# Kernel tuning notes

Measured on AMD Instinct MI355X. Metric: run time of the kernel, lower is better.

Reference implementation:

```python
import jax, jax.numpy as jnp
import numpy as np

GRID_RES = 96

TRIANGLE_TABLE = jnp.array([
    [-1, -1, -1, -1, -1, -1], [1, 0, 2, -1, -1, -1], [4, 0, 3, -1, -1, -1], [1, 4, 2, 1, 3, 4],
    [3, 1, 5, -1, -1, -1], [2, 3, 0, 2, 5, 3], [1, 4, 0, 1, 5, 4], [4, 2, 5, -1, -1, -1],
    [4, 5, 2, -1, -1, -1], [4, 1, 0, 4, 5, 1], [3, 2, 0, 3, 5, 2], [1, 3, 5, -1, -1, -1],
    [4, 1, 2, 4, 3, 1], [3, 0, 4, -1, -1, -1], [2, 0, 1, -1, -1, -1], [-1, -1, -1, -1, -1, -1]],
    dtype=jnp.int32)
NUM_TRIANGLES_TABLE = jnp.array([0, 1, 1, 2, 1, 2, 2, 1, 1, 2, 2, 1, 2, 1, 1, 0], dtype=jnp.int32)
BASE_TET_EDGES = jnp.array([0, 1, 0, 2, 0, 3, 1, 2, 1, 3, 2, 3], dtype=jnp.int32)


def _build_tet_grid(R):
    # vertices on an (R+1)^3 lattice spanning [-0.5, 0.5]^3
    n = R + 1
    lin = np.linspace(-0.5, 0.5, n, dtype=np.float32)
    X, Y, Z = np.meshgrid(lin, lin, lin, indexing='ij')
    verts = np.stack([X, Y, Z], axis=-1).reshape(-1, 3)
    idx = np.arange(n ** 3, dtype=np.int32).reshape(n, n, n)
    corners = []
    for dx in (0, 1):
        for dy in (0, 1):
            for dz in (0, 1):
                corners.append(idx[dx:dx + R, dy:dy + R, dz:dz + R].reshape(-1))
    c = np.stack(corners, axis=-1)  # (R^3, 8); corner bit order = dx*4 + dy*2 + dz
    SIX_TETS = np.array([[0, 5, 1, 7], [0, 1, 3, 7], [0, 3, 2, 7],
                         [0, 2, 6, 7], [0, 6, 4, 7], [0, 4, 5, 7]], dtype=np.int32)
    tets = c[:, SIX_TETS].reshape(-1, 4)  # (6*R^3, 4)
    return verts, tets


def _map_uv(face_gidx, max_idx):
    N = int(np.ceil(np.sqrt((max_idx + 1) // 2)))
    lin = jnp.linspace(0.0, 1.0 - 1.0 / N, N, dtype=jnp.float32)
    tex_y, tex_x = jnp.meshgrid(lin, lin, indexing='ij')
    pad = 0.9 / N
    uvs = jnp.stack([tex_x, tex_y, tex_x + pad, tex_y,
                     tex_x + pad, tex_y + pad, tex_x, tex_y + pad], axis=-1).reshape(-1, 2)
    tq = face_gidx // 2
    tet_idx = (tq // N) * N + (tq % N)
    tri_idx = face_gidx % 2
    uv_idx = jnp.stack([tet_idx * 4, tet_idx * 4 + tri_idx + 1, tet_idx * 4 + tri_idx + 2],
                       axis=-1).reshape(-1, 3)
    return uvs, uv_idx


def setup_inputs() -> dict:
    verts_np, tets_np = _build_tet_grid(GRID_RES)
    key = jax.random.key(0)
    verts = jnp.asarray(verts_np)
    noise = jax.random.normal(key, (verts.shape[0],), dtype=jnp.float32) * 0.02
    sdf_n = 0.35 - jnp.linalg.norm(verts, axis=-1) + noise  # sphere SDF + noise
    # 6 features per vertex: deformed position (xyz) + color (rgb=0.5), as in getMesh
    pos_nx3 = jnp.concatenate([verts, jnp.full(verts.shape, 0.5, dtype=jnp.float32)], axis=-1)
    return {"pos_nx3": pos_nx3, "sdf_n": sdf_n, "tet_fx4": jnp.asarray(tets_np)}


def reference(pos_nx3, sdf_n, tet_fx4):
    occ_n = sdf_n >= 0
    occ_fx4 = occ_n[tet_fx4]                       # (F, 4)
    occ_sum = occ_fx4.sum(-1)
    valid = (occ_sum > 0) & (occ_sum < 4)
    vt = tet_fx4[valid]                            # (T, 4) surface-crossing tets

    all_edges = vt[:, BASE_TET_EDGES].reshape(-1, 2)
    all_edges = jnp.sort(all_edges, axis=1)        # == sort_edges (min, max)
    unique_edges, idx_map = jnp.unique(all_edges, axis=0, return_inverse=True)
    idx_map = idx_map.reshape(-1)

    mask_edges = occ_n[unique_edges].sum(-1) == 1  # sign-crossing edges
    # mapping[mask] = arange(num_crossing); else -1 (cumsum assigns in sorted order)
    mapping = jnp.where(mask_edges, jnp.cumsum(mask_edges.astype(jnp.int32)) - 1, -1)
    idx_map = mapping[idx_map].reshape(-1, 6)      # (T, 6)
    interp_v = unique_edges[mask_edges]            # (Nv, 2)

    e_pos = pos_nx3[interp_v]                      # (Nv, 2, 6)
    e_sdf = sdf_n[interp_v] * jnp.array([1.0, -1.0], dtype=sdf_n.dtype)  # negate 2nd
    denom = e_sdf.sum(1, keepdims=True)            # (Nv, 1)
    w = jnp.flip(e_sdf, axis=1) / denom            # (Nv, 2) interpolation weights
    verts = (e_pos * w[..., None]).sum(1)          # (Nv, 6)

    v_id = jnp.array([1, 2, 4, 8], dtype=jnp.int32)
    tetindex = (occ_fx4[valid].astype(jnp.int32) * v_id).sum(-1)
    num_tri = NUM_TRIANGLES_TABLE[tetindex]
    tt = TRIANGLE_TABLE[tetindex]
    m1 = num_tri == 1
    m2 = num_tri == 2
    faces1 = jnp.take_along_axis(idx_map[m1], tt[m1][:, :3], axis=1).reshape(-1, 3)
    faces2 = jnp.take_along_axis(idx_map[m2], tt[m2][:, :6], axis=1).reshape(-1, 3)
    faces = jnp.concatenate([faces1, faces2], axis=0)

    num_tets = tet_fx4.shape[0]
    tet_gidx = jnp.arange(num_tets, dtype=jnp.int32)[valid]
    g2 = tet_gidx[m2] * 2
    face_gidx = jnp.concatenate([tet_gidx[m1] * 2,
                                 jnp.stack([g2, g2 + 1], axis=-1).reshape(-1)], axis=0)
    uvs, uv_idx = _map_uv(face_gidx, num_tets * 2)
    return verts, faces, uvs, uv_idx
```

## Files before the change

### kernel.cpp

```cpp
#include <hip/hip_runtime.h>
#include <stdint.h>

#define N1     97
#define N1SQ   9409
#define NV3    912673
#define RES    96
#define NCELL  884736
#define NCOLS  9409
#define COLS_PER_BLK 8
#define NBLK1  1177
#define SEG    2
#define UVFLOATS 42467328

#define VB2 3566
#define FB2 3456
#define NSPARSE (VB2 + FB2)
#define UVB2 10368
#define P2BLOCKS (2 * NSPARSE + (UVB2 - NSPARSE))

typedef float f4v __attribute__((ext_vector_type(4)));

__device__ __constant__ int d_tt[16][6] = {
    {-1,-1,-1,-1,-1,-1}, {1,0,2,-1,-1,-1}, {4,0,3,-1,-1,-1}, {1,4,2,1,3,4},
    {3,1,5,-1,-1,-1}, {2,3,0,2,5,3}, {1,4,0,1,5,4}, {4,2,5,-1,-1,-1},
    {4,5,2,-1,-1,-1}, {4,1,0,4,5,1}, {3,2,0,3,5,2}, {1,3,5,-1,-1,-1},
    {4,1,2,4,3,1}, {3,0,4,-1,-1,-1}, {2,0,1,-1,-1,-1}, {-1,-1,-1,-1,-1,-1}};
__device__ __constant__ int d_six[6][4] = {
    {0,5,1,7},{0,1,3,7},{0,3,2,7},{0,2,6,7},{0,6,4,7},{0,4,5,7}};
__device__ __constant__ int d_eb[6][2] = {{0,1},{0,2},{0,3},{1,2},{1,3},{2,3}};
__device__ __constant__ int d_diroff[7] = {1, 97, 98, 9409, 9410, 9506, 9507};

__device__ __forceinline__ int corner_off(int b) {
    return (b >> 2) * N1SQ + ((b >> 1) & 1) * N1 + (b & 1);
}

__device__ __forceinline__ float uvval(uint32_t p) {
    uint32_t cell = p >> 3;
    uint32_t k = p & 7u;
    uint32_t i = cell / 2304u;
    uint32_t j = cell - i * 2304u;
    uint32_t idx = (k & 1u) ? i : j;
    bool addpad = (k & 1u) ? (k >= 5u) : (k == 2u || k == 4u);
    return (float)idx * (1.0f / 2304.0f) + (addpad ? 0.9f / 2304.0f : 0.0f);
}

__global__ __launch_bounds__(1024) void k_p1(const float* __restrict__ sdf,
                                             uint8_t* __restrict__ mask,
                                             uint16_t* __restrict__ vloc,
                                             uint32_t* __restrict__ vsums,
                                             uint8_t* __restrict__ cocc,
                                             uint32_t* __restrict__ cloc,
                                             uint64_t* __restrict__ csums) {
    __shared__ uint8_t  sgn[COLS_PER_BLK][128];
    __shared__ uint64_t wtc[16];
    int t = threadIdx.x;
    int lane = t & 63, wv = t >> 6;
    int bid = blockIdx.x;
    int sub = t >> 7, z = t & 127;
    int col = bid * COLS_PER_BLK + sub;
    bool vcol = col < NCOLS;
    int x = 0, y = 0;
    if (vcol) { x = col / N1; y = col - x * N1; }
    bool bx = x < RES, by = y < RES, bz = z < RES;
    bool vact = vcol && (z < N1);
    int b00 = col * N1;
    float f00 = 0.f, f01 = 0.f, f10 = 0.f, f11 = 0.f;
    if (vact) {
        f00 = sdf[b00 + z];
        if (by) f01 = sdf[b00 + N1 + z];
        if (bx) f10 = sdf[b00 + N1SQ + z];
        if (bx && by) f11 = sdf[b00 + N1SQ + N1 + z];
    }
    uint32_t sb = (f00 >= 0.f ? 1u : 0u) | (f01 >= 0.f ? 2u : 0u) |
                  (f10 >= 0.f ? 4u : 0u) | (f11 >= 0.f ? 8u : 0u);
    sgn[sub][z] = (uint8_t)sb;
    __syncthreads();
    uint32_t s1 = bz ? (uint32_t)sgn[sub][z + 1] : 0u;

    uint32_t o0 = sb & 1u;
    uint32_t vm = 0;
    if (vact) {
        if (bz && ((s1 & 1u) != o0)) vm |= 1u;
        if (by && (((sb >> 1) & 1u) != o0)) vm |= 2u;
        if (by && bz && (((s1 >> 1) & 1u) != o0)) vm |= 4u;
        if (bx && (((sb >> 2) & 1u) != o0)) vm |= 8u;
        if (bx && bz && (((s1 >> 2) & 1u) != o0)) vm |= 16u;
        if (bx && by && (((sb >> 3) & 1u) != o0)) vm |= 32u;
        if (bx && by && bz && (((s1 >> 3) & 1u) != o0)) vm |= 64u;
    }
    uint32_t cnt = __popc(vm);
    bool cact = vact && bx && by && bz;
    uint32_t occ = 0, m1 = 0, m2 = 0;
    if (cact) {
        occ = (sb & 1u) | ((s1 & 1u) << 1) | (((sb >> 1) & 1u) << 2) | (((s1 >> 1) & 1u) << 3) |
              (((sb >> 2) & 1u) << 4) | (((s1 >> 2) & 1u) << 5) |
              (((sb >> 3) & 1u) << 6) | (((s1 >> 3) & 1u) << 7);
        if (occ != 0u && occ != 255u) {
#pragma unroll
            for (int k = 0; k < 6; k++) {
                int ti = ((occ >> d_six[k][0]) & 1) | (((occ >> d_six[k][1]) & 1) << 1) |
                         (((occ >> d_six[k][2]) & 1) << 2) | (((occ >> d_six[k][3]) & 1) << 3);
                int pc = __popc((uint32_t)ti);
                m1 += (pc == 1 || pc == 3) ? 1u : 0u;
                m2 += (pc == 2) ? 1u : 0u;
            }
        }
    }
    uint64_t val = (uint64_t)(cnt | (m1 << 16)) | ((uint64_t)m2 << 32);
    unsigned long long incl = val;
#pragma unroll
    for (int d = 1; d < 64; d <<= 1) {
        unsigned long long u = __shfl_up(incl, d, 64);
        if (lane >= d) incl += u;
    }
    if (lane == 63) wtc[wv] = incl;
    __syncthreads();
    uint64_t pre = 0;
#pragma unroll
    for (int w = 0; w < 16; w++)
        if (w < wv) pre += wtc[w];
    uint64_t excl = pre + (uint64_t)incl - val;

    if (vact) {
        mask[b00 + z] = (uint8_t)vm;
        vloc[b00 + z] = (uint16_t)(excl & 0xffffu);
    }
    if (cact) {
        int c = (x * RES + y) * RES + z;
        cocc[c] = (uint8_t)occ;
        cloc[c] = (uint32_t)((excl >> 16) & 0xffffu) | ((uint32_t)((excl >> 32) & 0xffffu) << 16);
    }
    if (t == 0) {
        uint64_t btot = 0;
#pragma unroll
        for (int w = 0; w < 16; w++) btot += wtc[w];
        vsums[bid] = (uint32_t)(btot & 0xffffu);
        csums[bid] = ((btot >> 16) & 0xffffu) | (((btot >> 32) & 0xffffu) << 32);
    }
}

__global__ __launch_bounds__(1024) void k_sums2(uint32_t* __restrict__ vsums,
                                                uint64_t* __restrict__ csums,
                                                uint32_t* __restrict__ tot) {
    __shared__ uint32_t wtv[16];
    __shared__ uint64_t wtc[16];
    int t = threadIdx.x;
    int lane = t & 63, wv = t >> 6;
    uint32_t sv = 0; uint64_t sc = 0;
    int base = t * SEG;
#pragma unroll
    for (int j = 0; j < SEG; j++) {
        int idx = base + j;
        if (idx < NBLK1) { sv += vsums[idx]; sc += csums[idx]; }
    }
    uint32_t iv = sv; unsigned long long ic = sc;
#pragma unroll
    for (int d = 1; d < 64; d <<= 1) {
        uint32_t u1 = __shfl_up(iv, d, 64);
        unsigned long long u2 = __shfl_up(ic, d, 64);
        if (lane >= d) { iv += u1; ic += u2; }
    }
    if (lane == 63) { wtv[wv] = iv; wtc[wv] = ic; }
    __syncthreads();
    uint32_t pv = 0; uint64_t pc2 = 0;
#pragma unroll
    for (int w = 0; w < 16; w++)
        if (w < wv) { pv += wtv[w]; pc2 += wtc[w]; }
    uint32_t rv = pv + iv - sv;
    uint64_t rc = pc2 + (uint64_t)ic - sc;
#pragma unroll
    for (int j = 0; j < SEG; j++) {
        int idx = base + j;
        if (idx < NBLK1) {
            uint32_t a = vsums[idx]; uint64_t b = csums[idx];
            vsums[idx] = rv; csums[idx] = rc;
            rv += a; rc += b;
        }
    }
    if (t == 0) {
        uint32_t NV = 0; uint64_t tc = 0;
#pragma unroll
        for (int w = 0; w < 16; w++) { NV += wtv[w]; tc += wtc[w]; }
        uint32_t NF1 = (uint32_t)(tc & 0xffffffffu);
        uint32_t NF2 = (uint32_t)(tc >> 32);
        uint32_t NF  = NF1 + 2u * NF2;
        tot[0] = NV; tot[1] = NF1; tot[2] = NF2;
        tot[3] = NV * 6u;
        tot[4] = NV * 6u + NF * 3u;
        tot[5] = NV * 6u + NF * 3u + UVFLOATS;
    }
}

__global__ __launch_bounds__(256) void k_p2(const float* __restrict__ sdf,
                                            const float* __restrict__ pos,
                                            const uint8_t* __restrict__ mask,
                                            const uint16_t* __restrict__ vloc,
                                            const uint32_t* __restrict__ vsums,
                                            const uint8_t* __restrict__ cocc,
                                            const uint32_t* __restrict__ cloc,
                                            const uint64_t* __restrict__ csums,
                                            const uint32_t* __restrict__ tot,
                                            float* __restrict__ out) {
    __shared__ uint2 ls[4][768];
    int bid = blockIdx.x;
    int t = threadIdx.x;
    int lane = t & 63, wv = t >> 6;
    int sparse = -1, uvb = -1;
    if (bid < 2 * NSPARSE) {
        if (bid & 1) uvb = bid >> 1;
        else sparse = bid >> 1;
    } else {
        uvb = NSPARSE + (bid - 2 * NSPARSE);
    }

    if (uvb >= 0) {
        uint32_t tot4 = tot[4];
        uint32_t A = (tot4 + 3u) & ~3u;
        uint32_t end = tot4 + UVFLOATS;
        uint32_t nvec = (end - A) >> 2;
        uint32_t vi0 = (uint32_t)uvb * 1024u + (uint32_t)t;
        uint32_t p0 = (A - tot4) + vi0 * 4u;
        uint32_t cell = p0 >> 3;
        uint32_t ph4 = p0 & 4u;
        uint32_t i = cell / 2304u;
        uint32_t j = cell - i * 2304u;
        const float s = 1.0f / 2304.0f, pd = 0.9f / 2304.0f;
#pragma unroll
        for (int rr = 0; rr < 4; rr++) {
            uint32_t vi = vi0 + (uint32_t)rr * 256u;
            if (vi < nvec) {
                float xx = (float)j * s, yy = (float)i * s;
                f4v val;
                if (ph4) { val.x = xx + pd; val.y = yy + pd; val.z = xx;      val.w = yy + pd; }
                else     { val.x = xx;      val.y = yy;      val.z = xx + pd; val.w = yy; }
                *(f4v*)(out + A + (size_t)vi * 4u) = val;
            }
            j += 128u;
            if (j >= 2304u) { j -= 2304u; i += 1u; }
        }
        if (uvb == 0 && t == 0) {
            for (uint32_t e = tot4; e < A; e++) out[e] = uvval(e - tot4);
            for (uint32_t e = A + nvec * 4u; e < end; e++) out[e] = uvval(e - tot4);
        }
        return;
    }

    if (sparse < VB2) {
        int v = sparse * 256 + wv * 64 + lane;
        uint32_t m = (v < NV3) ? (uint32_t)mask[v] : 0u;
        uint32_t cnt = __popc(m);
        uint32_t incl = cnt;
#pragma unroll
        for (int d = 1; d < 64; d <<= 1) {
            uint32_t u = __shfl_up(incl, d, 64);
            if (lane >= d) incl += u;
        }
        uint32_t E = __shfl(incl, 63);
        if (E == 0) return;
        uint32_t slot = incl - cnt;
        if (cnt) {
            uint32_t gvid = (uint32_t)vloc[v] + vsums[(v / N1) >> 3];
#pragma unroll
            for (int d = 0; d < 7; d++) {
                if ((m >> d) & 1u) {
                    ls[wv][slot] = make_uint2((uint32_t)v, (gvid << 3) | (uint32_t)d);
                    gvid++; slot++;
                }
            }
        }
        for (uint32_t j = lane; j < E; j += 64) {
            uint2 e = ls[wv][j];
            uint32_t v0 = e.x;
            uint32_t dir = e.y & 7u;
            uint32_t vid = e.y >> 3;
            uint32_t b = v0 + (uint32_t)d_diroff[dir];
            float sa = sdf[v0];
            float sbv = sdf[b];
            float inv = 1.0f / (sa - sbv);
            float w0 = -sbv * inv;
            float w1 = sa * inv;
            const float2* pa2 = (const float2*)(pos + (size_t)v0 * 6);
            const float2* pb2 = (const float2*)(pos + (size_t)b * 6);
            float2* o2 = (float2*)(out + (size_t)vid * 6);
#pragma unroll
            for (int k = 0; k < 3; k++) {
                float2 a = pa2[k], bb = pb2[k];
                float2 o;
                o.x = a.x * w0 + bb.x * w1;
                o.y = a.y * w0 + bb.y * w1;
                o2[k] = o;
            }
        }
        return;
    }

    {
        int c = (sparse - VB2) * 256 + wv * 64 + lane;
        uint32_t occ = cocc[c];
        bool valid = (occ != 0u && occ != 255u);
        uint32_t NF1 = tot[1];
        uint32_t tis = 0, nts = 0, cnt = 0;
        if (valid) {
#pragma unroll
            for (int k = 0; k < 6; k++) {
                int ti = ((occ >> d_six[k][0]) & 1) | (((occ >> d_six[k][1]) & 1) << 1) |
                         (((occ >> d_six[k][2]) & 1) << 2) | (((occ >> d_six[k][3]) & 1) << 3);
                int pc = __popc((uint32_t)ti);
                int nt = (pc == 2) ? 2 : ((pc == 1 || pc == 3) ? 1 : 0);
                tis |= (uint32_t)ti << (4 * k);
                nts |= (uint32_t)nt << (2 * k);
                cnt += (uint32_t)nt;
            }
        }
        uint32_t incl = cnt;
#pragma unroll
        for (int d = 1; d < 64; d <<= 1) {
            uint32_t u = __shfl_up(incl, d, 64);
            if (lane >= d) incl += u;
        }
        uint32_t E = __shfl(incl, 63);
        if (E == 0) return;
        uint32_t slot = incl - cnt;
        if (cnt) {
            uint32_t cl = cloc[c];
            uint64_t cs = csums[(((c / (RES * RES)) * N1) + ((c / RES) % RES)) >> 3];
            uint32_t r1 = (uint32_t)(cs & 0xffffffffu) + (cl & 0xffffu);
            uint32_t r2 = (uint32_t)(cs >> 32) + (cl >> 16);
#pragma unroll 1
            for (int k = 0; k < 6; k++) {
                uint32_t nt = (nts >> (2 * k)) & 3u;
                if (!nt) continue;
                uint32_t ti = (tis >> (4 * k)) & 15u;
                uint32_t row0;
                if (nt == 1) { row0 = r1; r1++; }
                else         { row0 = NF1 + 2u * r2; r2++; }
                for (uint32_t tri = 0; tri < nt; tri++) {
                    ls[wv][slot] = make_uint2((uint32_t)c,
                        ((row0 + tri) << 8) | (ti << 4) | ((uint32_t)k << 1) | tri);
                    slot++;
                }
            }
        }
        uint32_t fbase = tot[3];
        uint32_t ubase = tot[5];
        for (uint32_t j = lane; j < E; j += 64) {
            uint2 e = ls[wv][j];
            uint32_t cc = e.x;
            uint32_t tri = e.y & 1u;
            uint32_t k = (e.y >> 1) & 7u;
            uint32_t ti = (e.y >> 4) & 15u;
            uint32_t rr = e.y >> 8;
            uint32_t cx = cc / (RES * RES);
            uint32_t r0 = cc - cx * (RES * RES);
            uint32_t cy = r0 / RES;
            uint32_t cz = r0 - cy * RES;
            int base = (int)(cx * N1SQ + cy * N1 + cz);
            float* f = out + (size_t)fbase + (size_t)rr * 3;
            float* u = out + (size_t)ubase + (size_t)rr * 3;
#pragma unroll
            for (int jj = 0; jj < 3; jj++) {
                int ee = d_tt[ti][tri * 3 + jj];
                int c0 = d_six[k][d_eb[ee][0]];
                int c1 = d_six[k][d_eb[ee][1]];
                int bl = c0 & c1;
                int rank = (c0 ^ c1) - 1;
                int v0 = base + corner_off(bl);
                uint32_t vid = (uint32_t)vloc[v0] + vsums[(v0 / N1) >> 3] +
                               (uint32_t)__popc((uint32_t)mask[v0] & ((1u << rank) - 1u));
                f[jj] = (float)vid;
            }
            uint32_t t_g = cc * 6u + k;
            u[0] = (float)(4u * t_g);
            u[1] = (float)(4u * t_g + tri + 1u);
            u[2] = (float)(4u * t_g + tri + 2u);
        }
    }
}

extern "C" void kernel_launch(void* const* d_in, const int* in_sizes, int n_in,
                              void* d_out, int out_size, void* d_ws, size_t ws_size,
                              hipStream_t stream) {
    const float* pos = (const float*)d_in[0];
    const float* sdf = (const float*)d_in[1];
    float* out = (float*)d_out;

    uint8_t* ws = (uint8_t*)d_ws;
    size_t off = 0;
    auto alloc = [&](size_t bytes) {
        void* p = ws + off;
        off = (off + bytes + 255) & ~(size_t)255;
        return p;
    };
    uint32_t* tot   = (uint32_t*)alloc(64);
    uint8_t*  mask  = (uint8_t*)alloc(NV3);
    uint16_t* vloc  = (uint16_t*)alloc((size_t)NV3 * 2);
    uint32_t* vsums = (uint32_t*)alloc((size_t)NBLK1 * 4);
    uint8_t*  cocc  = (uint8_t*)alloc(NCELL);
    uint32_t* cloc  = (uint32_t*)alloc((size_t)NCELL * 4);
    uint64_t* csums = (uint64_t*)alloc((size_t)NBLK1 * 8);

    hipLaunchKernelGGL(k_p1, dim3(NBLK1), dim3(1024), 0, stream,
                       sdf, mask, vloc, vsums, cocc, cloc, csums);
    hipLaunchKernelGGL(k_sums2, dim3(1), dim3(1024), 0, stream, vsums, csums, tot);
    hipLaunchKernelGGL(k_p2, dim3(P2BLOCKS), dim3(256), 0, stream,
                       sdf, pos, mask, vloc, vsums, cocc, cloc, csums, tot, out);
}
```

Before: 57.19 us.

## Fuse block-sum scan into first pass via last-block atomic and pack mask/vloc

Removes the separate single-block scan kernel by having the last k_p1 block to finish (detected with an atomic counter) perform the block-sum prefix scan and totals. The vertex mask and local index are packed into one 32-bit word so the second pass gathers them with a single load. This adds a memset of the counter before launch and grows per-vertex storage from 3 to 4 bytes. Correctness relies on the acq_rel atomic making other blocks' sums visible.

New measurement: 95.32 us. 1.67x slower.

```diff
diff --git a/kernel.cpp b/kernel.cpp
--- a/kernel.cpp
+++ b/kernel.cpp
@@ -45,14 +45,17 @@
 }
 
 __global__ __launch_bounds__(1024) void k_p1(const float* __restrict__ sdf,
-                                             uint8_t* __restrict__ mask,
-                                             uint16_t* __restrict__ vloc,
+                                             uint32_t* __restrict__ mvl,
                                              uint32_t* __restrict__ vsums,
                                              uint8_t* __restrict__ cocc,
                                              uint32_t* __restrict__ cloc,
-                                             uint64_t* __restrict__ csums) {
+                                             uint64_t* __restrict__ csums,
+                                             uint32_t* __restrict__ tot,
+                                             uint32_t* __restrict__ ctl) {
     __shared__ uint8_t  sgn[COLS_PER_BLK][128];
     __shared__ uint64_t wtc[16];
+    __shared__ uint32_t wtv[16];
+    __shared__ uint32_t s_last;
     int t = threadIdx.x;
     int lane = t & 63, wv = t >> 6;
     int bid = blockIdx.x;
@@ -122,8 +125,7 @@
     uint64_t excl = pre + (uint64_t)incl - val;
 
     if (vact) {
-        mask[b00 + z] = (uint8_t)vm;
-        vloc[b00 + z] = (uint16_t)(excl & 0xffffu);
+        mvl[b00 + z] = ((uint32_t)(excl & 0xffffu) << 8) | vm;
     }
     if (cact) {
         int c = (x * RES + y) * RES + z;
@@ -137,64 +139,64 @@
         vsums[bid] = (uint32_t)(btot & 0xffffu);
         csums[bid] = ((btot >> 16) & 0xffffu) | (((btot >> 32) & 0xffffu) << 32);
     }
-}
-
-__global__ __launch_bounds__(1024) void k_sums2(uint32_t* __restrict__ vsums,
-                                                uint64_t* __restrict__ csums,
-                                                uint32_t* __restrict__ tot) {
-    __shared__ uint32_t wtv[16];
-    __shared__ uint64_t wtc[16];
-    int t = threadIdx.x;
-    int lane = t & 63, wv = t >> 6;
-    uint32_t sv = 0; uint64_t sc = 0;
-    int base = t * SEG;
-#pragma unroll
-    for (int j = 0; j < SEG; j++) {
-        int idx = base + j;
-        if (idx < NBLK1) { sv += vsums[idx]; sc += csums[idx]; }
-    }
-    uint32_t iv = sv; unsigned long long ic = sc;
-#pragma unroll
-    for (int d = 1; d < 64; d <<= 1) {
-        uint32_t u1 = __shfl_up(iv, d, 64);
-        unsigned long long u2 = __shfl_up(ic, d, 64);
-        if (lane >= d) { iv += u1; ic += u2; }
-    }
-    if (lane == 63) { wtv[wv] = iv; wtc[wv] = ic; }
     __syncthreads();
-    uint32_t pv = 0; uint64_t pc2 = 0;
-#pragma unroll
-    for (int w = 0; w < 16; w++)
-        if (w < wv) { pv += wtv[w]; pc2 += wtc[w]; }
-    uint32_t rv = pv + iv - sv;
-    uint64_t rc = pc2 + (uint64_t)ic - sc;
-#pragma unroll
-    for (int j = 0; j < SEG; j++) {
-        int idx = base + j;
-        if (idx < NBLK1) {
-            uint32_t a = vsums[idx]; uint64_t b = csums[idx];
-            vsums[idx] = rv; csums[idx] = rc;
-            rv += a; rc += b;
-        }
-    }
     if (t == 0) {
-        uint32_t NV = 0; uint64_t tc = 0;
-#pragma unroll
-        for (int w = 0; w < 16; w++) { NV += wtv[w]; tc += wtc[w]; }
-        uint32_t NF1 = (uint32_t)(tc & 0xffffffffu);
-        uint32_t NF2 = (uint32_t)(tc >> 32);
-        uint32_t NF  = NF1 + 2u * NF2;
-        tot[0] = NV; tot[1] = NF1; tot[2] = NF2;
-        tot[3] = NV * 6u;
-        tot[4] = NV * 6u + NF * 3u;
-        tot[5] = NV * 6u + NF * 3u + UVFLOATS;
+        uint32_t d = __hip_atomic_fetch_add(&ctl[0], 1u, __ATOMIC_ACQ_REL, __HIP_MEMORY_SCOPE_AGENT);
+        s_last = (d == NBLK1 - 1) ? 1u : 0u;
+    }
+    __syncthreads();
+    if (!s_last) return;
+
+    {
+        uint32_t sv = 0; uint64_t sc = 0;
+        int base = t * SEG;
+#pragma unroll
+        for (int j = 0; j < SEG; j++) {
+            int idx = base + j;
+            if (idx < NBLK1) { sv += vsums[idx]; sc += csums[idx]; }
+        }
+        uint32_t iv = sv; unsigned long long ic = sc;
+#pragma unroll
+        for (int d = 1; d < 64; d <<= 1) {
+            uint32_t u1 = __shfl_up(iv, d, 64);
+            unsigned long long u2 = __shfl_up(ic, d, 64);
+            if (lane >= d) { iv += u1; ic += u2; }
+        }
+        if (lane == 63) { wtv[wv] = iv; wtc[wv] = ic; }
+        __syncthreads();
+        uint32_t pv = 0; uint64_t pc2 = 0;
+#pragma unroll
+        for (int w = 0; w < 16; w++)
+            if (w < wv) { pv += wtv[w]; pc2 += wtc[w]; }
+        uint32_t rv = pv + iv - sv;
+        uint64_t rc = pc2 + (uint64_t)ic - sc;
+#pragma unroll
+        for (int j = 0; j < SEG; j++) {
+            int idx = base + j;
+            if (idx < NBLK1) {
+                uint32_t a = vsums[idx]; uint64_t b = csums[idx];
+                vsums[idx] = rv; csums[idx] = rc;
+                rv += a; rc += b;
+            }
+        }
+        if (t == 0) {
+            uint32_t NV = 0; uint64_t tc = 0;
+#pragma unroll
+            for (int w = 0; w < 16; w++) { NV += wtv[w]; tc += wtc[w]; }
+            uint32_t NF1 = (uint32_t)(tc & 0xffffffffu);
+            uint32_t NF2 = (uint32_t)(tc >> 32);
+            uint32_t NF  = NF1 + 2u * NF2;
+            tot[0] = NV; tot[1] = NF1; tot[2] = NF2;
+            tot[3] = NV * 6u;
+            tot[4] = NV * 6u + NF * 3u;
+            tot[5] = NV * 6u + NF * 3u + UVFLOATS;
+        }
     }
 }
 
 __global__ __launch_bounds__(256) void k_p2(const float* __restrict__ sdf,
                                             const float* __restrict__ pos,
-                                            const uint8_t* __restrict__ mask,
-                                            const uint16_t* __restrict__ vloc,
+                                            const uint32_t* __restrict__ mvl,
                                             const uint32_t* __restrict__ vsums,
                                             const uint8_t* __restrict__ cocc,
                                             const uint32_t* __restrict__ cloc,
@@ -247,7 +249,8 @@
 
     if (sparse < VB2) {
         int v = sparse * 256 + wv * 64 + lane;
-        uint32_t m = (v < NV3) ? (uint32_t)mask[v] : 0u;
+        uint32_t mv = (v < NV3) ? mvl[v] : 0u;
+        uint32_t m = mv & 0xffu;
         uint32_t cnt = __popc(m);
         uint32_t incl = cnt;
 #pragma unroll
@@ -259,7 +262,7 @@
         if (E == 0) return;
         uint32_t slot = incl - cnt;
         if (cnt) {
-            uint32_t gvid = (uint32_t)vloc[v] + vsums[(v / N1) >> 3];
+            uint32_t gvid = (mv >> 8) + vsums[(v / N1) >> 3];
 #pragma unroll
             for (int d = 0; d < 7; d++) {
                 if ((m >> d) & 1u) {
@@ -365,8 +368,9 @@
                 int bl = c0 & c1;
                 int rank = (c0 ^ c1) - 1;
                 int v0 = base + corner_off(bl);
-                uint32_t vid = (uint32_t)vloc[v0] + vsums[(v0 / N1) >> 3] +
-                               (uint32_t)__popc((uint32_t)mask[v0] & ((1u << rank) - 1u));
+                uint32_t mvlv = mvl[v0];
+                uint32_t vid = (mvlv >> 8) + vsums[(v0 / N1) >> 3] +
+                               (uint32_t)__popc((mvlv & 0xffu) & ((1u << rank) - 1u));
                 f[jj] = (float)vid;
             }
             uint32_t t_g = cc * 6u + k;
@@ -391,17 +395,17 @@
         off = (off + bytes + 255) & ~(size_t)255;
         return p;
     };
+    uint32_t* ctl   = (uint32_t*)alloc(64);
     uint32_t* tot   = (uint32_t*)alloc(64);
-    uint8_t*  mask  = (uint8_t*)alloc(NV3);
-    uint16_t* vloc  = (uint16_t*)alloc((size_t)NV3 * 2);
+    uint32_t* mvl   = (uint32_t*)alloc((size_t)NV3 * 4);
     uint32_t* vsums = (uint32_t*)alloc((size_t)NBLK1 * 4);
     uint8_t*  cocc  = (uint8_t*)alloc(NCELL);
     uint32_t* cloc  = (uint32_t*)alloc((size_t)NCELL * 4);
     uint64_t* csums = (uint64_t*)alloc((size_t)NBLK1 * 8);
 
+    hipMemsetAsync(ctl, 0, 64, stream);
     hipLaunchKernelGGL(k_p1, dim3(NBLK1), dim3(1024), 0, stream,
-                       sdf, mask, vloc, vsums, cocc, cloc, csums);
-    hipLaunchKernelGGL(k_sums2, dim3(1), dim3(1024), 0, stream, vsums, csums, tot);
+                       sdf, mvl, vsums, cocc, cloc, csums, tot, ctl);
     hipLaunchKernelGGL(k_p2, dim3(P2BLOCKS), dim3(256), 0, stream,
-                       sdf, pos, mask, vloc, vsums, cocc, cloc, csums, tot, out);
+                       sdf, pos, mvl, vsums, cocc, cloc, csums, tot, out);
 }
```
